# Performance work log

Measured on AMD Instinct MI355X. Metric: run time of the kernel, lower is better.

Reference implementation:

```python
import jax, jax.numpy as jnp
import numpy as np
from jax import lax

INP = 512
OUT = 512
T = 2048
B = 64


def setup_inputs() -> dict:
    key = jax.random.key(0)
    ks = jax.random.split(key, 7)
    rang = (1.0 / OUT) ** 0.5
    u = lambda k, shape: jax.random.uniform(k, shape, jnp.float32, -rang, rang)
    return {
        "x": jax.random.normal(ks[0], (T, B, INP), jnp.float32),
        "g": u(ks[1], (INP, OUT)),
        "gb": u(ks[2], (OUT,)),
        "h": u(ks[3], (INP, OUT)),
        "hb": u(ks[4], (OUT,)),
        "r": u(ks[5], (1, OUT)),
        "rb": u(ks[6], (OUT,)),
    }


def reference(x, g, gb, h, hb, r, rb):
    # x: [T, B, inp]
    Tn = x.shape[0]
    # time gate: r_t = 2*sigmoid((n/T) * r + rb), shape [T, out]
    t = (jnp.arange(Tn, dtype=x.dtype) / Tn)[:, None]  # [T, 1]
    rt = 2.0 * jax.nn.sigmoid(t * r[0] + rb)           # [T, out]
    # precompute per-step gates (vectorized over T)
    G = jax.nn.sigmoid(jnp.einsum("tbi,io->tbo", x, g) + gb) * rt[:, None, :]
    H = jnp.tanh(jnp.einsum("tbi,io->tbo", x, h) + hb) * rt[:, None, :]

    def step(y, gh):
        g_t, h_t = gh
        return y * g_t + h_t, None

    y0 = jnp.zeros((x.shape[1], x.shape[2] * 0 + G.shape[-1]), dtype=x.dtype)
    y, _ = lax.scan(step, y0, (G, H))
    return y
```

## Files before the change

### kernel.cpp

```cpp
#include <hip/hip_runtime.h>
#include <cstdint>
#include <cstddef>

#define TT   2048
#define BB   64
#define KK   512
#define OO   512
#define NCH  64
#define TC   32

typedef __attribute__((ext_vector_type(8))) short short8;
typedef __attribute__((ext_vector_type(4))) float f32x4;

__device__ __forceinline__ unsigned short f2bf(float f) {
  unsigned int u = __float_as_uint(f);
  unsigned int rounding = 0x7FFFu + ((u >> 16) & 1u);
  return (unsigned short)((u + rounding) >> 16);
}

__device__ __forceinline__ float sigmoid_f(float z) {
  return 1.0f / (1.0f + __expf(-z));
}

__device__ __forceinline__ float tanh_f(float z) {
  z = fminf(15.0f, fmaxf(-15.0f, z));
  float e = __expf(-2.0f * z);
  return (1.0f - e) / (1.0f + e);
}

__device__ __forceinline__ void async_ld16(const void* g, void* l) {
  __builtin_amdgcn_global_load_lds(
      (const __attribute__((address_space(1))) void*)g,
      (__attribute__((address_space(3))) void*)l, 16, 0, 0);
}

__global__ void convert_x_k(const float4* __restrict__ x4,
                            ushort4* __restrict__ xb4, int n4) {
  int i = blockIdx.x * blockDim.x + threadIdx.x;
  int stride = gridDim.x * blockDim.x;
  for (; i < n4; i += stride) {
    float4 v = x4[i];
    ushort4 o;
    o.x = f2bf(v.x); o.y = f2bf(v.y); o.z = f2bf(v.z); o.w = f2bf(v.w);
    xb4[i] = o;
  }
}

__global__ void prep_weights_k(const float* __restrict__ g,
                               const float* __restrict__ h,
                               unsigned short* __restrict__ Gt,
                               unsigned short* __restrict__ Ht) {
  __shared__ float tile[32][33];
  const float* src = (blockIdx.z == 0) ? g : h;
  unsigned short* dst = (blockIdx.z == 0) ? Gt : Ht;
  int ox = blockIdx.x * 32;
  int ky = blockIdx.y * 32;
  int tx = threadIdx.x, ty = threadIdx.y;
  #pragma unroll
  for (int r = ty; r < 32; r += 8)
    tile[r][tx] = src[(ky + r) * OO + ox + tx];
  __syncthreads();
  #pragma unroll
  for (int r = ty; r < 32; r += 8)
    dst[(size_t)(ox + r) * KK + ky + tx] = f2bf(tile[tx][r]);
}

__global__ __launch_bounds__(512, 2) void rnn_fused3_k(
    const unsigned short* __restrict__ xb,
    const unsigned short* __restrict__ Gt,
    const unsigned short* __restrict__ Ht,
    const float* __restrict__ gb, const float* __restrict__ hb,
    const float* __restrict__ r,  const float* __restrict__ rb,
    float* __restrict__ chunkA, float* __restrict__ chunkB) {
  extern __shared__ __align__(16) unsigned short smem[];

  const int tid  = threadIdx.x;
  const int wave = tid >> 6;
  const int lane = tid & 63;
  const int quad = lane >> 4;
  const int lcol = lane & 15;

  const int bi = blockIdx.x;
  const int ot = bi >> 6;
  const int c  = bi & 63;
  const int o  = ot * 128 + wave * 16 + lcol;

  const float gbv = gb[o], hbv = hb[o];
  const float rv  = r[o],  rbv = rb[o];

  short8 Bg[8][2], Bh[8][2];
  {
    const unsigned short* gp = Gt + (size_t)o * KK + quad * 8;
    const unsigned short* hp = Ht + (size_t)o * KK + quad * 8;
    #pragma unroll
    for (int kc = 0; kc < 8; ++kc)
      #pragma unroll
      for (int ks = 0; ks < 2; ++ks) {
        Bg[kc][ks] = *(const short8*)(gp + kc * 64 + ks * 32);
        Bh[kc][ks] = *(const short8*)(hp + kc * 64 + ks * 32);
      }
  }

  auto stage = [&](int trow, int buf) {
    unsigned short* dst = smem + buf * 32768 + wave * 8 * 512;
    const unsigned short* src = xb + ((size_t)trow * BB + wave * 8) * KK;
    #pragma unroll
    for (int rr = 0; rr < 8; ++rr) {
      int gch = (lane & ~7) | ((lane & 7) ^ rr);
      async_ld16(src + rr * KK + gch * 8, dst + rr * 512);
    }
  };

  stage(c * TC, 0);

  float SA[16], SB[16];
  #pragma unroll
  for (int s = 0; s < 16; s++) { SA[s] = 1.0f; SB[s] = 0.0f; }

  f32x4 accG[4], accH[4];
  #pragma unroll
  for (int m = 0; m < 4; m++) {
    f32x4 z = {0.0f, 0.0f, 0.0f, 0.0f};
    accG[m] = z; accH[m] = z;
  }

  __syncthreads();

  int p = 0;
  for (int it = 0; it < TC; ++it) {
    if (it + 1 < TC) stage(c * TC + it + 1, p ^ 1);

    const unsigned short* A0 = smem + p * 32768;
    #pragma unroll
    for (int kc = 0; kc < 8; ++kc)
      #pragma unroll
      for (int ks = 0; ks < 2; ++ks)
        #pragma unroll
        for (int mt = 0; mt < 4; ++mt) {
          int arow = mt * 16 + lcol;
          int slot = kc * 8 + ((ks * 4 + quad) ^ (arow & 7));
          short8 a = *(const short8*)(A0 + arow * 512 + slot * 8);
          accG[mt] = __builtin_amdgcn_mfma_f32_16x16x32_bf16(
              a, Bg[kc][ks], accG[mt], 0, 0, 0);
          accH[mt] = __builtin_amdgcn_mfma_f32_16x16x32_bf16(
              a, Bh[kc][ks], accH[mt], 0, 0, 0);
        }

    const int t = c * TC + it;
    const float rt = 2.0f * sigmoid_f(((float)t * (1.0f / TT)) * rv + rbv);
    #pragma unroll
    for (int mt = 0; mt < 4; ++mt)
      #pragma unroll
      for (int reg = 0; reg < 4; ++reg) {
        float G = sigmoid_f(accG[mt][reg] + gbv) * rt;
        float H = tanh_f  (accH[mt][reg] + hbv) * rt;
        int s = mt * 4 + reg;
        SB[s] = fmaf(G, SB[s], H);
        SA[s] *= G;
        accG[mt][reg] = 0.0f;
        accH[mt][reg] = 0.0f;
      }

    __syncthreads();
    p ^= 1;
  }

  #pragma unroll
  for (int mt = 0; mt < 4; ++mt)
    #pragma unroll
    for (int reg = 0; reg < 4; ++reg) {
      int s = mt * 4 + reg;
      int b = mt * 16 + quad * 4 + reg;
      size_t idx = ((size_t)c * BB + b) * OO + o;
      chunkA[idx] = SA[s];
      chunkB[idx] = SB[s];
    }
}

__global__ void combine_k(const float* __restrict__ cA,
                          const float* __restrict__ cB,
                          float* __restrict__ out) {
  int i = blockIdx.x * blockDim.x + threadIdx.x;
  float y = 0.0f;
  #pragma unroll 8
  for (int c = 0; c < NCH; c++) {
    float A  = cA[(size_t)c * (BB * OO) + i];
    float Bv = cB[(size_t)c * (BB * OO) + i];
    y = fmaf(A, y, Bv);
  }
  out[i] = y;
}

extern "C" void kernel_launch(void* const* d_in, const int* in_sizes, int n_in,
                              void* d_out, int out_size, void* d_ws, size_t ws_size,
                              hipStream_t stream) {
  (void)in_sizes; (void)n_in; (void)out_size; (void)ws_size;
  const float* x  = (const float*)d_in[0];
  const float* g  = (const float*)d_in[1];
  const float* gb = (const float*)d_in[2];
  const float* h  = (const float*)d_in[3];
  const float* hb = (const float*)d_in[4];
  const float* r  = (const float*)d_in[5];
  const float* rb = (const float*)d_in[6];
  float* out = (float*)d_out;

  char* w = (char*)d_ws;
  unsigned short* xb = (unsigned short*)w;
  unsigned short* Gt = (unsigned short*)(w + 134217728);
  unsigned short* Ht = (unsigned short*)(w + 134742016);
  float* chunkA = (float*)(w + 135266304);
  float* chunkB = (float*)(w + 143654912);

  static bool attr_set = false;
  if (!attr_set) {
    hipFuncSetAttribute(reinterpret_cast<const void*>(rnn_fused3_k),
                        hipFuncAttributeMaxDynamicSharedMemorySize, 131072);
    attr_set = true;
  }

  const int n4 = (TT * BB * KK) / 4;
  convert_x_k<<<8192, 256, 0, stream>>>((const float4*)x, (ushort4*)xb, n4);
  prep_weights_k<<<dim3(16, 16, 2), dim3(32, 8), 0, stream>>>(g, h, Gt, Ht);
  rnn_fused3_k<<<NCH * 4, 512, 131072, stream>>>(xb, Gt, Ht, gb, hb, r, rb,
                                                 chunkA, chunkB);
  combine_k<<<(BB * OO) / 256, 256, 0, stream>>>(chunkA, chunkB, out);
}
```

Before: 538.4 us.

## Fuse fp32-to-bf16 conversion of x into main kernel with split register prefetch

Removes the separate conversion kernel and the bf16 copy of x. The main kernel now loads fp32 x into registers, converts it and writes bf16 into LDS. The prefetch is split into two halves interleaved with the MFMA loop so the load latency overlaps compute. This trades a full extra pass over x for double the global read bytes inside the main kernel and higher register pressure.

```diff
diff --git a/kernel.cpp b/kernel.cpp
--- a/kernel.cpp
+++ b/kernel.cpp
@@ -26,24 +26,6 @@
   z = fminf(15.0f, fmaxf(-15.0f, z));
   float e = __expf(-2.0f * z);
   return (1.0f - e) / (1.0f + e);
-}
-
-__device__ __forceinline__ void async_ld16(const void* g, void* l) {
-  __builtin_amdgcn_global_load_lds(
-      (const __attribute__((address_space(1))) void*)g,
-      (__attribute__((address_space(3))) void*)l, 16, 0, 0);
-}
-
-__global__ void convert_x_k(const float4* __restrict__ x4,
-                            ushort4* __restrict__ xb4, int n4) {
-  int i = blockIdx.x * blockDim.x + threadIdx.x;
-  int stride = gridDim.x * blockDim.x;
-  for (; i < n4; i += stride) {
-    float4 v = x4[i];
-    ushort4 o;
-    o.x = f2bf(v.x); o.y = f2bf(v.y); o.z = f2bf(v.z); o.w = f2bf(v.w);
-    xb4[i] = o;
-  }
 }
 
 __global__ void prep_weights_k(const float* __restrict__ g,
@@ -66,7 +48,7 @@
 }
 
 __global__ __launch_bounds__(512, 2) void rnn_fused3_k(
-    const unsigned short* __restrict__ xb,
+    const float* __restrict__ x,
     const unsigned short* __restrict__ Gt,
     const unsigned short* __restrict__ Ht,
     const float* __restrict__ gb, const float* __restrict__ hb,
@@ -101,17 +83,38 @@
       }
   }
 
-  auto stage = [&](int trow, int buf) {
+  auto issue4 = [&](int trow, int half, f32x4 (&v)[4][2]) {
+    const float* src = x + ((size_t)trow * BB + wave * 8) * KK;
+    #pragma unroll
+    for (int j = 0; j < 4; ++j) {
+      int rr = half * 4 + j;
+      int gch = (lane & ~7) | ((lane & 7) ^ rr);
+      const float* p0 = src + (size_t)rr * KK + (size_t)gch * 8;
+      v[j][0] = *(const f32x4*)(p0);
+      v[j][1] = *(const f32x4*)(p0 + 4);
+    }
+  };
+  auto write4 = [&](int buf, int half, f32x4 (&v)[4][2]) {
     unsigned short* dst = smem + buf * 32768 + wave * 8 * 512;
-    const unsigned short* src = xb + ((size_t)trow * BB + wave * 8) * KK;
-    #pragma unroll
-    for (int rr = 0; rr < 8; ++rr) {
-      int gch = (lane & ~7) | ((lane & 7) ^ rr);
-      async_ld16(src + rr * KK + gch * 8, dst + rr * 512);
+    #pragma unroll
+    for (int j = 0; j < 4; ++j) {
+      int rr = half * 4 + j;
+      short8 w;
+      #pragma unroll
+      for (int e = 0; e < 4; ++e) w[e]     = (short)f2bf(v[j][0][e]);
+      #pragma unroll
+      for (int e = 0; e < 4; ++e) w[4 + e] = (short)f2bf(v[j][1][e]);
+      *(short8*)(dst + rr * 512 + lane * 8) = w;
     }
   };
 
-  stage(c * TC, 0);
+  {
+    f32x4 s0[4][2], s1[4][2];
+    issue4(c * TC, 0, s0);
+    issue4(c * TC, 1, s1);
+    write4(0, 0, s0);
+    write4(0, 1, s1);
+  }
 
   float SA[16], SB[16];
   #pragma unroll
@@ -128,11 +131,14 @@
 
   int p = 0;
   for (int it = 0; it < TC; ++it) {
-    if (it + 1 < TC) stage(c * TC + it + 1, p ^ 1);
+    const bool pref = (it + 1 < TC);
+    f32x4 st[4][2];
+
+    if (pref) issue4(c * TC + it + 1, 0, st);
 
     const unsigned short* A0 = smem + p * 32768;
     #pragma unroll
-    for (int kc = 0; kc < 8; ++kc)
+    for (int kc = 0; kc < 4; ++kc)
       #pragma unroll
       for (int ks = 0; ks < 2; ++ks)
         #pragma unroll
@@ -146,6 +152,26 @@
               a, Bh[kc][ks], accH[mt], 0, 0, 0);
         }
 
+    if (pref) {
+      write4(p ^ 1, 0, st);
+      issue4(c * TC + it + 1, 1, st);
+    }
+
+    #pragma unroll
+    for (int kc = 4; kc < 8; ++kc)
+      #pragma unroll
+      for (int ks = 0; ks < 2; ++ks)
+        #pragma unroll
+        for (int mt = 0; mt < 4; ++mt) {
+          int arow = mt * 16 + lcol;
+          int slot = kc * 8 + ((ks * 4 + quad) ^ (arow & 7));
+          short8 a = *(const short8*)(A0 + arow * 512 + slot * 8);
+          accG[mt] = __builtin_amdgcn_mfma_f32_16x16x32_bf16(
+              a, Bg[kc][ks], accG[mt], 0, 0, 0);
+          accH[mt] = __builtin_amdgcn_mfma_f32_16x16x32_bf16(
+              a, Bh[kc][ks], accH[mt], 0, 0, 0);
+        }
+
     const int t = c * TC + it;
     const float rt = 2.0f * sigmoid_f(((float)t * (1.0f / TT)) * rv + rbv);
     #pragma unroll
@@ -160,6 +186,8 @@
         accG[mt][reg] = 0.0f;
         accH[mt][reg] = 0.0f;
       }
+
+    if (pref) write4(p ^ 1, 1, st);
 
     __syncthreads();
     p ^= 1;
@@ -205,11 +233,10 @@
   float* out = (float*)d_out;
 
   char* w = (char*)d_ws;
-  unsigned short* xb = (unsigned short*)w;
-  unsigned short* Gt = (unsigned short*)(w + 134217728);
-  unsigned short* Ht = (unsigned short*)(w + 134742016);
-  float* chunkA = (float*)(w + 135266304);
-  float* chunkB = (float*)(w + 143654912);
+  unsigned short* Gt = (unsigned short*)w;
+  unsigned short* Ht = (unsigned short*)(w + 524288);
+  float* chunkA = (float*)(w + 1048576);
+  float* chunkB = (float*)(w + 9437184);
 
   static bool attr_set = false;
   if (!attr_set) {
@@ -218,10 +245,8 @@
     attr_set = true;
   }
 
-  const int n4 = (TT * BB * KK) / 4;
-  convert_x_k<<<8192, 256, 0, stream>>>((const float4*)x, (ushort4*)xb, n4);
   prep_weights_k<<<dim3(16, 16, 2), dim3(32, 8), 0, stream>>>(g, h, Gt, Ht);
-  rnn_fused3_k<<<NCH * 4, 512, 131072, stream>>>(xb, Gt, Ht, gb, hb, r, rb,
+  rnn_fused3_k<<<NCH * 4, 512, 131072, stream>>>(x, Gt, Ht, gb, hb, r, rb,
                                                  chunkA, chunkB);
   combine_k<<<(BB * OO) / 256, 256, 0, stream>>>(chunkA, chunkB, out);
 }
```

Result: slower. 584.8 us (+8.6%).

## Split x staging into half-K stages with 4-deep async pipeline and vmcnt waits

Applied to the files above, without the earlier changes.

The per-timestep x tile is now loaded as two half-K stages into a ring of four LDS buffers, with three stages kept in flight. A fine-grained s_waitcnt vmcnt plus a raw s_barrier replaces the full __syncthreads double-buffer. MFMA sections run at raised wave priority. The aim is to hide global-to-LDS load latency behind the matrix work and cut barrier stalls, at the cost of more fragile hand-counted vmcnt synchronisation.

```diff
diff --git a/kernel.cpp b/kernel.cpp
--- a/kernel.cpp
+++ b/kernel.cpp
@@ -65,7 +65,7 @@
     dst[(size_t)(ox + r) * KK + ky + tx] = f2bf(tile[tx][r]);
 }
 
-__global__ __launch_bounds__(512, 2) void rnn_fused3_k(
+__global__ __launch_bounds__(512, 2) void rnn_fused4_k(
     const unsigned short* __restrict__ xb,
     const unsigned short* __restrict__ Gt,
     const unsigned short* __restrict__ Ht,
@@ -88,34 +88,35 @@
   const float gbv = gb[o], hbv = hb[o];
   const float rv  = r[o],  rbv = rb[o];
 
-  short8 Bg[8][2], Bh[8][2];
+  short8 Bg[16], Bh[16];
   {
     const unsigned short* gp = Gt + (size_t)o * KK + quad * 8;
     const unsigned short* hp = Ht + (size_t)o * KK + quad * 8;
     #pragma unroll
-    for (int kc = 0; kc < 8; ++kc)
-      #pragma unroll
-      for (int ks = 0; ks < 2; ++ks) {
-        Bg[kc][ks] = *(const short8*)(gp + kc * 64 + ks * 32);
-        Bh[kc][ks] = *(const short8*)(hp + kc * 64 + ks * 32);
-      }
-  }
-
-  auto stage = [&](int trow, int buf) {
-    unsigned short* dst = smem + buf * 32768 + wave * 8 * 512;
-    const unsigned short* src = xb + ((size_t)trow * BB + wave * 8) * KK;
-    #pragma unroll
-    for (int rr = 0; rr < 8; ++rr) {
-      int gch = (lane & ~7) | ((lane & 7) ^ rr);
-      async_ld16(src + rr * KK + gch * 8, dst + rr * 512);
+    for (int K16 = 0; K16 < 16; ++K16) {
+      Bg[K16] = *(const short8*)(gp + K16 * 32);
+      Bh[K16] = *(const short8*)(hp + K16 * 32);
+    }
+  }
+
+  auto stage = [&](int s) {
+    unsigned short* dst = smem + (s & 3) * 16384 + wave * 2048;
+    const int t = c * TC + (s >> 1);
+    const unsigned short* srcb = xb + (size_t)t * (BB * KK) + (s & 1) * 256;
+    #pragma unroll
+    for (int j = 0; j < 4; ++j) {
+      int rr  = 2 * j + (lane >> 5);
+      int gch = (lane & 31) ^ rr;
+      async_ld16(srcb + (size_t)(wave * 8 + rr) * KK + gch * 8,
+                 dst + j * 512);
     }
   };
 
-  stage(c * TC, 0);
+  stage(0); stage(1); stage(2);
 
   float SA[16], SB[16];
   #pragma unroll
-  for (int s = 0; s < 16; s++) { SA[s] = 1.0f; SB[s] = 0.0f; }
+  for (int s2 = 0; s2 < 16; ++s2) { SA[s2] = 1.0f; SB[s2] = 0.0f; }
 
   f32x4 accG[4], accH[4];
   #pragma unroll
@@ -124,56 +125,67 @@
     accG[m] = z; accH[m] = z;
   }
 
-  __syncthreads();
-
-  int p = 0;
-  for (int it = 0; it < TC; ++it) {
-    if (it + 1 < TC) stage(c * TC + it + 1, p ^ 1);
-
-    const unsigned short* A0 = smem + p * 32768;
-    #pragma unroll
-    for (int kc = 0; kc < 8; ++kc)
+  for (int t = 0; t < TC; ++t) {
+    const int b0 = (t & 1) * 2;
+    #pragma unroll
+    for (int h = 0; h < 2; ++h) {
+      if (t < TC - 1) {
+        asm volatile("s_waitcnt vmcnt(8)" ::: "memory");
+      } else if (h == 0) {
+        asm volatile("s_waitcnt vmcnt(4)" ::: "memory");
+      } else {
+        asm volatile("s_waitcnt vmcnt(0)" ::: "memory");
+      }
+      __builtin_amdgcn_sched_barrier(0);
+      __builtin_amdgcn_s_barrier();
+
+      const int sn = 2 * t + h + 3;
+      if (sn < 2 * TC) stage(sn);
+
+      const unsigned short* A0 = smem + (b0 + h) * 16384;
+      __builtin_amdgcn_s_setprio(1);
       #pragma unroll
-      for (int ks = 0; ks < 2; ++ks)
+      for (int k2 = 0; k2 < 8; ++k2) {
+        const int K16 = h * 8 + k2;
         #pragma unroll
         for (int mt = 0; mt < 4; ++mt) {
-          int arow = mt * 16 + lcol;
-          int slot = kc * 8 + ((ks * 4 + quad) ^ (arow & 7));
-          short8 a = *(const short8*)(A0 + arow * 512 + slot * 8);
+          const int arow = mt * 16 + lcol;
+          const int sl   = (k2 * 4 + quad) ^ (lcol & 7);
+          short8 a = *(const short8*)(A0 + arow * 256 + sl * 8);
           accG[mt] = __builtin_amdgcn_mfma_f32_16x16x32_bf16(
-              a, Bg[kc][ks], accG[mt], 0, 0, 0);
+              a, Bg[K16], accG[mt], 0, 0, 0);
           accH[mt] = __builtin_amdgcn_mfma_f32_16x16x32_bf16(
-              a, Bh[kc][ks], accH[mt], 0, 0, 0);
+              a, Bh[K16], accH[mt], 0, 0, 0);
         }
-
-    const int t = c * TC + it;
-    const float rt = 2.0f * sigmoid_f(((float)t * (1.0f / TT)) * rv + rbv);
+      }
+      __builtin_amdgcn_s_setprio(0);
+    }
+
+    const int tt = c * TC + t;
+    const float rt = 2.0f * sigmoid_f(((float)tt * (1.0f / TT)) * rv + rbv);
     #pragma unroll
     for (int mt = 0; mt < 4; ++mt)
       #pragma unroll
       for (int reg = 0; reg < 4; ++reg) {
         float G = sigmoid_f(accG[mt][reg] + gbv) * rt;
         float H = tanh_f  (accH[mt][reg] + hbv) * rt;
-        int s = mt * 4 + reg;
-        SB[s] = fmaf(G, SB[s], H);
-        SA[s] *= G;
+        int s2 = mt * 4 + reg;
+        SB[s2] = fmaf(G, SB[s2], H);
+        SA[s2] *= G;
         accG[mt][reg] = 0.0f;
         accH[mt][reg] = 0.0f;
       }
-
-    __syncthreads();
-    p ^= 1;
   }
 
   #pragma unroll
   for (int mt = 0; mt < 4; ++mt)
     #pragma unroll
     for (int reg = 0; reg < 4; ++reg) {
-      int s = mt * 4 + reg;
+      int s2 = mt * 4 + reg;
       int b = mt * 16 + quad * 4 + reg;
       size_t idx = ((size_t)c * BB + b) * OO + o;
-      chunkA[idx] = SA[s];
-      chunkB[idx] = SB[s];
+      chunkA[idx] = SA[s2];
+      chunkB[idx] = SB[s2];
     }
 }
 
@@ -213,7 +225,7 @@
 
   static bool attr_set = false;
   if (!attr_set) {
-    hipFuncSetAttribute(reinterpret_cast<const void*>(rnn_fused3_k),
+    hipFuncSetAttribute(reinterpret_cast<const void*>(rnn_fused4_k),
                         hipFuncAttributeMaxDynamicSharedMemorySize, 131072);
     attr_set = true;
   }
@@ -221,7 +233,7 @@
   const int n4 = (TT * BB * KK) / 4;
   convert_x_k<<<8192, 256, 0, stream>>>((const float4*)x, (ushort4*)xb, n4);
   prep_weights_k<<<dim3(16, 16, 2), dim3(32, 8), 0, stream>>>(g, h, Gt, Ht);
-  rnn_fused3_k<<<NCH * 4, 512, 131072, stream>>>(xb, Gt, Ht, gb, hb, r, rb,
+  rnn_fused4_k<<<NCH * 4, 512, 131072, stream>>>(xb, Gt, Ht, gb, hb, r, rb,
                                                  chunkA, chunkB);
   combine_k<<<(BB * OO) / 256, 256, 0, stream>>>(chunkA, chunkB, out);
 }
```

Result: no change. 541.9 us (+0.6%).
